# Kernel optimization log

Hardware: AMD Instinct MI355X
Metric: run time of the kernel (lower is better)

## Reference

```python
import jax, jax.numpy as jnp
import numpy as np

N_T, D_MODEL, RANK, BATCH = 64, 1024, 8, 4096
THRESHOLD = 0.0  # jumprelu threshold (forward default)


def setup_inputs() -> dict:
    key = jax.random.key(0)
    k_x, k_v, k_u, k_e = jax.random.split(key, 4)
    scale = (1.0 / (D_MODEL * RANK)) ** 0.25
    x = jax.random.normal(k_x, (BATCH, D_MODEL), dtype=jnp.float32)
    V = jax.random.normal(k_v, (N_T, RANK, D_MODEL), dtype=jnp.float32) * scale
    U = jax.random.normal(k_u, (N_T, D_MODEL, RANK), dtype=jnp.float32) * scale
    encoder = jax.random.normal(k_e, (N_T, D_MODEL), dtype=jnp.float32)
    encoder = encoder / jnp.linalg.norm(encoder, axis=1, keepdims=True)
    bias = -jnp.ones((N_T,), dtype=jnp.float32)  # init_constant(bias, -1.0)
    return {"x": x, "V": V, "U": U, "encoder": encoder, "bias": bias}


def jumprelu(x, threshold=THRESHOLD):
    # forward: hard threshold x * 1[x > threshold]
    return x * (x > threshold).astype(x.dtype)


def reference(x, V, U, encoder, bias):
    # pre_acts: (batch, n)
    pre_acts = x @ encoder.T - bias
    gate = jumprelu(pre_acts)  # activation_fn='jumprelu', threshold=0.0
    # Vx: (n, batch, rank)
    Vx = jnp.einsum('nrd,bd->nbr', V, x)
    # UVx: (n, batch, d) -- the large intermediate a fused kernel would avoid
    UVx = jnp.einsum('ndr,nbr->nbd', U, Vx)
    # gated sum over transforms: (batch, d)
    output = jnp.einsum('nbd,bn->bd', UVx, gate)
    u_norms = jnp.linalg.norm(U.reshape(U.shape[0], -1), axis=1)
    v_norms = jnp.linalg.norm(V.reshape(V.shape[0], -1), axis=1)
    frobenius_norms = u_norms * v_norms / (D_MODEL * RANK) ** 0.5
    return output, gate, frobenius_norms
```

## Files before the change

kernel.cpp:

```cpp
#include <hip/hip_runtime.h>
#include <math.h>

#define BATCHN 4096
#define DMODEL 1024
#define NT 64
#define RANK 8
#define K2 512

typedef __attribute__((ext_vector_type(8))) short bf16x8;
typedef __attribute__((ext_vector_type(4))) float f32x4;

__device__ __forceinline__ void async16(void* lds, const void* g) {
    __builtin_amdgcn_global_load_lds(
        (const __attribute__((address_space(1))) void*)g,
        (__attribute__((address_space(3))) void*)lds, 16, 0, 0);
}

__device__ __forceinline__ short f2bf(float f) {
    unsigned u = __builtin_bit_cast(unsigned, f);
    u += 0x7fffu + ((u >> 16) & 1u);
    return (short)(u >> 16);
}

__global__ __launch_bounds__(256) void convert_kernel(
    const float* __restrict__ x, const float* __restrict__ enc,
    const float* __restrict__ V, const float* __restrict__ U,
    unsigned short* __restrict__ xb, unsigned short* __restrict__ Wb,
    unsigned short* __restrict__ Ub,
    float* __restrict__ su_part, float* __restrict__ sv_part)
{
    const int b = blockIdx.x, t = threadIdx.x;
    const float* src;
    unsigned short* dst;
    float* psum = nullptr;
    if (b < 2048) {
        const int e0 = b * 2048 + t * 8;
        src = x + e0; dst = xb + e0;
    } else if (b < 2336) {
        const int e0 = (b - 2048) * 2048 + t * 8;
        const int row = e0 >> 10, col = e0 & 1023;
        if (row < 64) {
            src = enc + (size_t)row * 1024 + col;
        } else {
            src = V + (size_t)(row - 64) * 1024 + col;
            const int vrow = (b - 2048) * 2 - 64;
            psum = sv_part + (vrow >> 3) * 4 + ((vrow & 7) >> 1);
        }
        dst = Wb + e0;
    } else {
        const int bi = b - 2336;
        const int e0 = bi * 2048 + t * 8;
        src = U + e0; dst = Ub + e0;
        psum = su_part + (bi >> 2) * 4 + (bi & 3);
    }
    float4 v0 = *(const float4*)src;
    float4 v1 = *(const float4*)(src + 4);
    bf16x8 o;
    o[0] = f2bf(v0.x); o[1] = f2bf(v0.y); o[2] = f2bf(v0.z); o[3] = f2bf(v0.w);
    o[4] = f2bf(v1.x); o[5] = f2bf(v1.y); o[6] = f2bf(v1.z); o[7] = f2bf(v1.w);
    *(bf16x8*)dst = o;

    if (psum) {
        float s = v0.x*v0.x + v0.y*v0.y + v0.z*v0.z + v0.w*v0.w
                + v1.x*v1.x + v1.y*v1.y + v1.z*v1.z + v1.w*v1.w;
        #pragma unroll
        for (int off = 32; off; off >>= 1) s += __shfl_down(s, off);
        __shared__ float red[4];
        if ((t & 63) == 0) red[t >> 6] = s;
        __syncthreads();
        if (t == 0) *psum = red[0] + red[1] + red[2] + red[3];
    }
}

__global__ __launch_bounds__(256) void gatevx_kernel(
    const unsigned short* __restrict__ A, const unsigned short* __restrict__ Bm,
    const float* __restrict__ bias,
    float* __restrict__ gate_out, unsigned short* __restrict__ vx_out)
{
    constexpr int BK = 128, KDIM = DMODEL;
    __shared__ unsigned short As[32 * BK];
    __shared__ unsigned short Bs[64 * BK];
    const int t = threadIdx.x;
    const int wave = t >> 6, lane = t & 63;
    const int bm = blockIdx.y, bn = blockIdx.x;
    const int wm = wave & 1, wn = wave >> 1;
    const int l15 = lane & 15, lq = lane >> 4;

    f32x4 acc[2] = {};
    const size_t Abase = (size_t)bm * 32 * KDIM;
    const size_t Bbase = (size_t)bn * 64 * KDIM;

    for (int k0 = 0; k0 < KDIM; k0 += BK) {
        #pragma unroll
        for (int c = 0; c < 2; ++c) {
            const int r0 = wave * 8 + c * 4;
            const int row = r0 + lq;
            const int g = l15 ^ (row & 15);
            async16(&As[r0 * BK], A + Abase + (size_t)row * KDIM + k0 + g * 8);
        }
        #pragma unroll
        for (int c = 0; c < 4; ++c) {
            const int r0 = wave * 16 + c * 4;
            const int row = r0 + lq;
            const int g = l15 ^ (row & 15);
            async16(&Bs[r0 * BK], Bm + Bbase + (size_t)row * KDIM + k0 + g * 8);
        }
        __syncthreads();
        #pragma unroll
        for (int s = 0; s < 4; ++s) {
            const int kc = s * 4 + lq;
            const int m = wm * 16 + l15;
            bf16x8 af = *(const bf16x8*)&As[m * BK + ((kc ^ (m & 15)) * 8)];
            bf16x8 bfr[2];
            #pragma unroll
            for (int j = 0; j < 2; ++j) {
                const int n = wn * 32 + j * 16 + l15;
                bfr[j] = *(const bf16x8*)&Bs[n * BK + ((kc ^ (n & 15)) * 8)];
            }
            #pragma unroll
            for (int j = 0; j < 2; ++j)
                acc[j] = __builtin_amdgcn_mfma_f32_16x16x32_bf16(
                    af, bfr[j], acc[j], 0, 0, 0);
        }
        __syncthreads();
    }

    const int rowb = bm * 32 + wm * 16 + lq * 4;
    #pragma unroll
    for (int j = 0; j < 2; ++j) {
        const int col = wn * 32 + j * 16 + l15;
        #pragma unroll
        for (int r = 0; r < 4; ++r) {
            const int row = rowb + r;
            const float v = acc[j][r];
            if (bn == 0) {
                const float p = v - bias[col];
                gate_out[(size_t)row * NT + col] = p > 0.f ? p : 0.f;
            } else {
                vx_out[(size_t)row * K2 + (bn - 1) * 64 + col] = (unsigned short)f2bf(v);
            }
        }
    }
}

__global__ __launch_bounds__(256) void out_kernel(
    const unsigned short* __restrict__ vx, const float* __restrict__ gate,
    const unsigned short* __restrict__ Ub, float* __restrict__ out,
    const float* __restrict__ su_part, const float* __restrict__ sv_part,
    float* __restrict__ fro)
{
    constexpr int BK = 128, KDIM = K2;
    __shared__ unsigned short As[64 * BK];
    __shared__ unsigned short Bs[16 * 64 * 8];
    const int t = threadIdx.x;
    const int wave = t >> 6, lane = t & 63;
    const int bm = blockIdx.y, bn = blockIdx.x;
    const int wm = wave & 1, wn = wave >> 1;
    const int l15 = lane & 15, lq = lane >> 4;

    f32x4 acc[2][2] = {};

    for (int k0 = 0; k0 < KDIM; k0 += BK) {
        const int nb = k0 >> 3;
        #pragma unroll
        for (int i = 0; i < 4; ++i) {
            const int row = wave * 16 + i * 4 + lq;
            const int grow = bm * 64 + row;
            const int g = l15 ^ (row & 15);
            bf16x8 v = *(const bf16x8*)(vx + (size_t)grow * K2 + k0 + g * 8);
            const float gs = gate[(size_t)grow * NT + nb + g];
            bf16x8 o;
            #pragma unroll
            for (int e = 0; e < 8; ++e) {
                const float f = __builtin_bit_cast(float,
                    ((unsigned)(unsigned short)v[e]) << 16);
                o[e] = (short)(__builtin_bit_cast(unsigned, f * gs) >> 16);
            }
            *(bf16x8*)&As[row * BK + l15 * 8] = o;
        }
        #pragma unroll
        for (int c = 0; c < 4; ++c) {
            const int kc = c * 4 + wave;
            async16(&Bs[kc * 512],
                    Ub + (size_t)(nb + kc) * (DMODEL * RANK)
                       + (size_t)(bn * 64 + lane) * RANK);
        }
        __syncthreads();
        #pragma unroll
        for (int s = 0; s < 4; ++s) {
            const int kc = s * 4 + lq;
            bf16x8 af[2], bfr[2];
            #pragma unroll
            for (int i = 0; i < 2; ++i) {
                const int m = wm * 32 + i * 16 + l15;
                af[i] = *(const bf16x8*)&As[m * BK + ((kc ^ (m & 15)) * 8)];
            }
            #pragma unroll
            for (int j = 0; j < 2; ++j) {
                const int n = wn * 32 + j * 16 + l15;
                bfr[j] = *(const bf16x8*)&Bs[kc * 512 + n * 8];
            }
            #pragma unroll
            for (int i = 0; i < 2; ++i)
                #pragma unroll
                for (int j = 0; j < 2; ++j)
                    acc[i][j] = __builtin_amdgcn_mfma_f32_16x16x32_bf16(
                        af[i], bfr[j], acc[i][j], 0, 0, 0);
        }
        __syncthreads();
    }

    #pragma unroll
    for (int i = 0; i < 2; ++i) {
        const int rowb = bm * 64 + wm * 32 + i * 16 + lq * 4;
        #pragma unroll
        for (int j = 0; j < 2; ++j) {
            const int col = bn * 64 + wn * 32 + j * 16 + l15;
            #pragma unroll
            for (int r = 0; r < 4; ++r)
                out[(size_t)(rowb + r) * DMODEL + col] = acc[i][j][r];
        }
    }

    if (bn == 0 && bm == 0 && t < NT) {
        float su = su_part[t * 4] + su_part[t * 4 + 1] + su_part[t * 4 + 2] + su_part[t * 4 + 3];
        float sv = sv_part[t * 4] + sv_part[t * 4 + 1] + sv_part[t * 4 + 2] + sv_part[t * 4 + 3];
        fro[t] = sqrtf(su) * sqrtf(sv) / sqrtf((float)(DMODEL * RANK));
    }
}

extern "C" void kernel_launch(void* const* d_in, const int* in_sizes, int n_in,
                              void* d_out, int out_size, void* d_ws, size_t ws_size,
                              hipStream_t stream) {
    const float* x    = (const float*)d_in[0];
    const float* V    = (const float*)d_in[1];
    const float* U    = (const float*)d_in[2];
    const float* enc  = (const float*)d_in[3];
    const float* bias = (const float*)d_in[4];

    float* out  = (float*)d_out;
    float* gate = out + (size_t)BATCHN * DMODEL;
    float* fro  = gate + (size_t)BATCHN * NT;

    char* ws = (char*)d_ws;
    unsigned short* xb = (unsigned short*)ws;
    unsigned short* Wb = (unsigned short*)(ws + 8388608);
    unsigned short* Ub = (unsigned short*)(ws + 9568256);
    unsigned short* vx = (unsigned short*)(ws + 10616832);
    float* su_part     = (float*)(ws + 14811136);
    float* sv_part     = (float*)(ws + 14812160);

    convert_kernel<<<2592, 256, 0, stream>>>(x, enc, V, U, xb, Wb, Ub, su_part, sv_part);
    gatevx_kernel<<<dim3(9, 128), 256, 0, stream>>>(xb, Wb, bias, gate, vx);
    out_kernel<<<dim3(16, 64), 256, 0, stream>>>(vx, gate, Ub, out, su_part, sv_part, fro);
}
```

Before: 109.1 us.

## Fuse fp32-to-bf16 conversion into GEMM loads and drop the convert kernel

Removes the separate conversion kernel: both GEMMs now read fp32 x, encoder, V and U directly and convert to bf16 while staging into LDS. The Frobenius norms move into extra blocks of the first GEMM launch. The first GEMM tile grows to 64x64, giving fewer blocks with more MFMA work each. The intent is to save one launch and the bf16 workspace round trip, at the cost of synchronous register-staged loads instead of async global-to-LDS copies, repeated conversion of x across 9 column blocks, and fp32 reads of U in every out_kernel block.

```diff
diff --git a/kernel.cpp b/kernel.cpp
--- a/kernel.cpp
+++ b/kernel.cpp
@@ -10,10 +10,9 @@
 typedef __attribute__((ext_vector_type(8))) short bf16x8;
 typedef __attribute__((ext_vector_type(4))) float f32x4;
 
-__device__ __forceinline__ void async16(void* lds, const void* g) {
-    __builtin_amdgcn_global_load_lds(
-        (const __attribute__((address_space(1))) void*)g,
-        (__attribute__((address_space(3))) void*)lds, 16, 0, 0);
+__device__ __forceinline__ short f2bf_hu(float f) {
+    unsigned u = __builtin_bit_cast(unsigned, f);
+    return (short)((u + 0x8000u) >> 16);
 }
 
 __device__ __forceinline__ short f2bf(float f) {
@@ -22,135 +21,118 @@
     return (short)(u >> 16);
 }
 
-__global__ __launch_bounds__(256) void convert_kernel(
-    const float* __restrict__ x, const float* __restrict__ enc,
-    const float* __restrict__ V, const float* __restrict__ U,
-    unsigned short* __restrict__ xb, unsigned short* __restrict__ Wb,
-    unsigned short* __restrict__ Ub,
-    float* __restrict__ su_part, float* __restrict__ sv_part)
+__device__ __forceinline__ bf16x8 cvt8(const float* __restrict__ p) {
+    float4 v0 = *(const float4*)p;
+    float4 v1 = *(const float4*)(p + 4);
+    bf16x8 o;
+    o[0] = f2bf_hu(v0.x); o[1] = f2bf_hu(v0.y); o[2] = f2bf_hu(v0.z); o[3] = f2bf_hu(v0.w);
+    o[4] = f2bf_hu(v1.x); o[5] = f2bf_hu(v1.y); o[6] = f2bf_hu(v1.z); o[7] = f2bf_hu(v1.w);
+    return o;
+}
+
+__global__ __launch_bounds__(256) void gatevx_norms_kernel(
+    const float* __restrict__ x, const float* __restrict__ V,
+    const float* __restrict__ U, const float* __restrict__ enc,
+    const float* __restrict__ bias,
+    float* __restrict__ gate, float* __restrict__ fro,
+    unsigned short* __restrict__ vx)
 {
-    const int b = blockIdx.x, t = threadIdx.x;
-    const float* src;
-    unsigned short* dst;
-    float* psum = nullptr;
-    if (b < 2048) {
-        const int e0 = b * 2048 + t * 8;
-        src = x + e0; dst = xb + e0;
-    } else if (b < 2336) {
-        const int e0 = (b - 2048) * 2048 + t * 8;
-        const int row = e0 >> 10, col = e0 & 1023;
-        if (row < 64) {
-            src = enc + (size_t)row * 1024 + col;
-        } else {
-            src = V + (size_t)(row - 64) * 1024 + col;
-            const int vrow = (b - 2048) * 2 - 64;
-            psum = sv_part + (vrow >> 3) * 4 + ((vrow & 7) >> 1);
-        }
-        dst = Wb + e0;
-    } else {
-        const int bi = b - 2336;
-        const int e0 = bi * 2048 + t * 8;
-        src = U + e0; dst = Ub + e0;
-        psum = su_part + (bi >> 2) * 4 + (bi & 3);
-    }
-    float4 v0 = *(const float4*)src;
-    float4 v1 = *(const float4*)(src + 4);
-    bf16x8 o;
-    o[0] = f2bf(v0.x); o[1] = f2bf(v0.y); o[2] = f2bf(v0.z); o[3] = f2bf(v0.w);
-    o[4] = f2bf(v1.x); o[5] = f2bf(v1.y); o[6] = f2bf(v1.z); o[7] = f2bf(v1.w);
-    *(bf16x8*)dst = o;
-
-    if (psum) {
-        float s = v0.x*v0.x + v0.y*v0.y + v0.z*v0.z + v0.w*v0.w
-                + v1.x*v1.x + v1.y*v1.y + v1.z*v1.z + v1.w*v1.w;
-        #pragma unroll
-        for (int off = 32; off; off >>= 1) s += __shfl_down(s, off);
-        __shared__ float red[4];
-        if ((t & 63) == 0) red[t >> 6] = s;
-        __syncthreads();
-        if (t == 0) *psum = red[0] + red[1] + red[2] + red[3];
-    }
-}
-
-__global__ __launch_bounds__(256) void gatevx_kernel(
-    const unsigned short* __restrict__ A, const unsigned short* __restrict__ Bm,
-    const float* __restrict__ bias,
-    float* __restrict__ gate_out, unsigned short* __restrict__ vx_out)
-{
-    constexpr int BK = 128, KDIM = DMODEL;
-    __shared__ unsigned short As[32 * BK];
-    __shared__ unsigned short Bs[64 * BK];
-    const int t = threadIdx.x;
+    __shared__ unsigned short As[64 * 128];
+    __shared__ unsigned short Bs[64 * 128];
+    __shared__ float red[8];
+    const int bid = blockIdx.x, t = threadIdx.x;
     const int wave = t >> 6, lane = t & 63;
-    const int bm = blockIdx.y, bn = blockIdx.x;
     const int wm = wave & 1, wn = wave >> 1;
     const int l15 = lane & 15, lq = lane >> 4;
 
-    f32x4 acc[2] = {};
-    const size_t Abase = (size_t)bm * 32 * KDIM;
-    const size_t Bbase = (size_t)bn * 64 * KDIM;
-
-    for (int k0 = 0; k0 < KDIM; k0 += BK) {
-        #pragma unroll
-        for (int c = 0; c < 2; ++c) {
-            const int r0 = wave * 8 + c * 4;
-            const int row = r0 + lq;
-            const int g = l15 ^ (row & 15);
-            async16(&As[r0 * BK], A + Abase + (size_t)row * KDIM + k0 + g * 8);
-        }
-        #pragma unroll
-        for (int c = 0; c < 4; ++c) {
-            const int r0 = wave * 16 + c * 4;
-            const int row = r0 + lq;
-            const int g = l15 ^ (row & 15);
-            async16(&Bs[r0 * BK], Bm + Bbase + (size_t)row * KDIM + k0 + g * 8);
-        }
+    if (bid < 576) {
+        const int bn = bid % 9, bm = bid / 9;
+        const float* Brow = (bn == 0) ? enc : (V + (size_t)(bn - 1) * 64 * DMODEL);
+        f32x4 acc[2][2] = {};
+        for (int k0 = 0; k0 < DMODEL; k0 += 128) {
+            #pragma unroll
+            for (int c = 0; c < 4; ++c) {
+                const int row = wave * 16 + c * 4 + lq;
+                const int g = l15 ^ (row & 15);
+                bf16x8 oa = cvt8(x + (size_t)(bm * 64 + row) * DMODEL + k0 + g * 8);
+                *(bf16x8*)&As[row * 128 + l15 * 8] = oa;
+                bf16x8 ob = cvt8(Brow + (size_t)row * DMODEL + k0 + g * 8);
+                *(bf16x8*)&Bs[row * 128 + l15 * 8] = ob;
+            }
+            __syncthreads();
+            #pragma unroll
+            for (int s = 0; s < 4; ++s) {
+                const int kc = s * 4 + lq;
+                bf16x8 af[2], bfr[2];
+                #pragma unroll
+                for (int i = 0; i < 2; ++i) {
+                    const int m = wm * 32 + i * 16 + l15;
+                    af[i] = *(const bf16x8*)&As[m * 128 + ((kc ^ (m & 15)) * 8)];
+                }
+                #pragma unroll
+                for (int j = 0; j < 2; ++j) {
+                    const int n = wn * 32 + j * 16 + l15;
+                    bfr[j] = *(const bf16x8*)&Bs[n * 128 + ((kc ^ (n & 15)) * 8)];
+                }
+                #pragma unroll
+                for (int i = 0; i < 2; ++i)
+                    #pragma unroll
+                    for (int j = 0; j < 2; ++j)
+                        acc[i][j] = __builtin_amdgcn_mfma_f32_16x16x32_bf16(
+                            af[i], bfr[j], acc[i][j], 0, 0, 0);
+            }
+            __syncthreads();
+        }
+        #pragma unroll
+        for (int i = 0; i < 2; ++i) {
+            const int rowb = bm * 64 + wm * 32 + i * 16 + lq * 4;
+            #pragma unroll
+            for (int j = 0; j < 2; ++j) {
+                const int col = wn * 32 + j * 16 + l15;
+                #pragma unroll
+                for (int r = 0; r < 4; ++r) {
+                    const int row = rowb + r;
+                    const float v = acc[i][j][r];
+                    if (bn == 0) {
+                        const float p = v - bias[col];
+                        gate[(size_t)row * NT + col] = p > 0.f ? p : 0.f;
+                    } else {
+                        vx[(size_t)row * K2 + (bn - 1) * 64 + col] = (unsigned short)f2bf(v);
+                    }
+                }
+            }
+        }
+    } else {
+        const int n = bid - 576;
+        const float* Up = U + (size_t)n * (DMODEL * RANK);
+        const float* Vp = V + (size_t)n * (DMODEL * RANK);
+        float su = 0.f, sv = 0.f;
+        for (int i = t * 4; i < DMODEL * RANK; i += 1024) {
+            float4 a = *(const float4*)(Up + i);
+            su += a.x * a.x + a.y * a.y + a.z * a.z + a.w * a.w;
+            float4 b = *(const float4*)(Vp + i);
+            sv += b.x * b.x + b.y * b.y + b.z * b.z + b.w * b.w;
+        }
+        #pragma unroll
+        for (int off = 32; off; off >>= 1) {
+            su += __shfl_down(su, off);
+            sv += __shfl_down(sv, off);
+        }
+        if ((t & 63) == 0) { red[wave * 2] = su; red[wave * 2 + 1] = sv; }
         __syncthreads();
-        #pragma unroll
-        for (int s = 0; s < 4; ++s) {
-            const int kc = s * 4 + lq;
-            const int m = wm * 16 + l15;
-            bf16x8 af = *(const bf16x8*)&As[m * BK + ((kc ^ (m & 15)) * 8)];
-            bf16x8 bfr[2];
-            #pragma unroll
-            for (int j = 0; j < 2; ++j) {
-                const int n = wn * 32 + j * 16 + l15;
-                bfr[j] = *(const bf16x8*)&Bs[n * BK + ((kc ^ (n & 15)) * 8)];
-            }
-            #pragma unroll
-            for (int j = 0; j < 2; ++j)
-                acc[j] = __builtin_amdgcn_mfma_f32_16x16x32_bf16(
-                    af, bfr[j], acc[j], 0, 0, 0);
-        }
-        __syncthreads();
-    }
-
-    const int rowb = bm * 32 + wm * 16 + lq * 4;
-    #pragma unroll
-    for (int j = 0; j < 2; ++j) {
-        const int col = wn * 32 + j * 16 + l15;
-        #pragma unroll
-        for (int r = 0; r < 4; ++r) {
-            const int row = rowb + r;
-            const float v = acc[j][r];
-            if (bn == 0) {
-                const float p = v - bias[col];
-                gate_out[(size_t)row * NT + col] = p > 0.f ? p : 0.f;
-            } else {
-                vx_out[(size_t)row * K2 + (bn - 1) * 64 + col] = (unsigned short)f2bf(v);
-            }
+        if (t == 0) {
+            float tu = red[0] + red[2] + red[4] + red[6];
+            float tv = red[1] + red[3] + red[5] + red[7];
+            fro[n] = sqrtf(tu) * sqrtf(tv) / sqrtf((float)(DMODEL * RANK));
         }
     }
 }
 
 __global__ __launch_bounds__(256) void out_kernel(
     const unsigned short* __restrict__ vx, const float* __restrict__ gate,
-    const unsigned short* __restrict__ Ub, float* __restrict__ out,
-    const float* __restrict__ su_part, const float* __restrict__ sv_part,
-    float* __restrict__ fro)
+    const float* __restrict__ U, float* __restrict__ out)
 {
-    constexpr int BK = 128, KDIM = K2;
-    __shared__ unsigned short As[64 * BK];
+    __shared__ unsigned short As[64 * 128];
     __shared__ unsigned short Bs[16 * 64 * 8];
     const int t = threadIdx.x;
     const int wave = t >> 6, lane = t & 63;
@@ -160,7 +142,7 @@
 
     f32x4 acc[2][2] = {};
 
-    for (int k0 = 0; k0 < KDIM; k0 += BK) {
+    for (int k0 = 0; k0 < K2; k0 += 128) {
         const int nb = k0 >> 3;
         #pragma unroll
         for (int i = 0; i < 4; ++i) {
@@ -176,14 +158,14 @@
                     ((unsigned)(unsigned short)v[e]) << 16);
                 o[e] = (short)(__builtin_bit_cast(unsigned, f * gs) >> 16);
             }
-            *(bf16x8*)&As[row * BK + l15 * 8] = o;
+            *(bf16x8*)&As[row * 128 + l15 * 8] = o;
         }
         #pragma unroll
         for (int c = 0; c < 4; ++c) {
             const int kc = c * 4 + wave;
-            async16(&Bs[kc * 512],
-                    Ub + (size_t)(nb + kc) * (DMODEL * RANK)
-                       + (size_t)(bn * 64 + lane) * RANK);
+            bf16x8 o = cvt8(U + (size_t)(nb + kc) * (DMODEL * RANK)
+                              + (size_t)(bn * 64 + lane) * RANK);
+            *(bf16x8*)&Bs[kc * 512 + lane * 8] = o;
         }
         __syncthreads();
         #pragma unroll
@@ -193,7 +175,7 @@
             #pragma unroll
             for (int i = 0; i < 2; ++i) {
                 const int m = wm * 32 + i * 16 + l15;
-                af[i] = *(const bf16x8*)&As[m * BK + ((kc ^ (m & 15)) * 8)];
+                af[i] = *(const bf16x8*)&As[m * 128 + ((kc ^ (m & 15)) * 8)];
             }
             #pragma unroll
             for (int j = 0; j < 2; ++j) {
@@ -220,12 +202,6 @@
             for (int r = 0; r < 4; ++r)
                 out[(size_t)(rowb + r) * DMODEL + col] = acc[i][j][r];
         }
-    }
-
-    if (bn == 0 && bm == 0 && t < NT) {
-        float su = su_part[t * 4] + su_part[t * 4 + 1] + su_part[t * 4 + 2] + su_part[t * 4 + 3];
-        float sv = sv_part[t * 4] + sv_part[t * 4 + 1] + sv_part[t * 4 + 2] + sv_part[t * 4 + 3];
-        fro[t] = sqrtf(su) * sqrtf(sv) / sqrtf((float)(DMODEL * RANK));
     }
 }
 
@@ -241,16 +217,8 @@
     float* out  = (float*)d_out;
     float* gate = out + (size_t)BATCHN * DMODEL;
     float* fro  = gate + (size_t)BATCHN * NT;
-
-    char* ws = (char*)d_ws;
-    unsigned short* xb = (unsigned short*)ws;
-    unsigned short* Wb = (unsigned short*)(ws + 8388608);
-    unsigned short* Ub = (unsigned short*)(ws + 9568256);
-    unsigned short* vx = (unsigned short*)(ws + 10616832);
-    float* su_part     = (float*)(ws + 14811136);
-    float* sv_part     = (float*)(ws + 14812160);
-
-    convert_kernel<<<2592, 256, 0, stream>>>(x, enc, V, U, xb, Wb, Ub, su_part, sv_part);
-    gatevx_kernel<<<dim3(9, 128), 256, 0, stream>>>(xb, Wb, bias, gate, vx);
-    out_kernel<<<dim3(16, 64), 256, 0, stream>>>(vx, gate, Ub, out, su_part, sv_part, fro);
-}
+    unsigned short* vx = (unsigned short*)d_ws;
+
+    gatevx_norms_kernel<<<640, 256, 0, stream>>>(x, V, U, enc, bias, gate, fro, vx);
+    out_kernel<<<dim3(16, 64), 256, 0, stream>>>(vx, gate, U, out);
+}
```

New measurement: 121.0 us. +10.9%, slower.
